# Optimization experiments

Measured on AMD Instinct MI355X. Metric: run time of the kernel, lower is better.

The kernel has to match this reference:

```python
import jax, jax.numpy as jnp
import numpy as np

D_MODEL = 128


def setup_inputs() -> dict:
    key = jax.random.key(0)
    ks = jax.random.split(key, 7)
    d = D_MODEL
    B, N = 4, 512
    # Kaiming-ish init scales for linear layers
    W1 = jax.random.normal(ks[0], (2 * d, d), jnp.float32) / np.sqrt(2 * d)
    b1 = jnp.zeros((d,), jnp.float32)
    W2 = jax.random.normal(ks[1], (d, d // 2), jnp.float32) / np.sqrt(d)
    b2 = jnp.zeros((d // 2,), jnp.float32)
    W3 = jax.random.normal(ks[2], (d // 2, 1), jnp.float32) / np.sqrt(d // 2)
    b3 = jnp.zeros((1,), jnp.float32)
    node_features = jax.random.normal(ks[3], (B, N, d), jnp.float32)
    return {"node_features": node_features, "W1": W1, "b1": b1,
            "W2": W2, "b2": b2, "W3": W3, "b3": b3}


def reference(node_features, W1, b1, W2, b2, W3, b3):
    # node_features: [B, N, d]. Pairwise concat [x_i, x_j] @ W1 is split as
    # x_i @ W1[:d] + x_j @ W1[d:] — same math as cat+Linear, but avoids
    # materializing the [B, N, N, 2d] concat tensor.
    d = node_features.shape[-1]
    hi = jnp.einsum('bnd,dk->bnk', node_features, W1[:d])   # [B, N, d]
    hj = jnp.einsum('bnd,dk->bnk', node_features, W1[d:])   # [B, N, d]
    h = jax.nn.relu(hi[:, :, None, :] + hj[:, None, :, :] + b1)  # [B, N, N, d]
    h = jax.nn.relu(jnp.einsum('bijk,km->bijm', h, W2) + b2)      # [B, N, N, d/2]
    logits = jnp.einsum('bijm,mo->bijo', h, W3) + b3              # [B, N, N, 1]
    return jax.nn.sigmoid(logits[..., 0])                          # [B, N, N]
```

## Files before the change

### kernel.cpp

```cpp
#include <hip/hip_runtime.h>
#include <hip/hip_fp16.h>

#define D_MODEL 128
#define NB 4
#define NN 512

typedef _Float16 f16;
typedef _Float16 f16x8 __attribute__((ext_vector_type(8)));
typedef float f32x4 __attribute__((ext_vector_type(4)));

__global__ __launch_bounds__(256) void prep_kernel(
    const float* __restrict__ x,
    const float* __restrict__ W1,
    const float* __restrict__ b1,
    const float* __restrict__ W2,
    f16* __restrict__ Hi, f16* __restrict__ Hj, f16* __restrict__ W2p)
{
    const int blk = blockIdx.x;
    const int t = threadIdx.x;
    if (blk < 256) {
        const int r0 = blk * 8;
        __shared__ float xs[8][128];
        for (int idx = t; idx < 8 * 128; idx += 256)
            xs[idx >> 7][idx & 127] = x[(size_t)r0 * 128 + idx];
        __syncthreads();

        const int isJ = t >> 7;
        const int k = t & 127;
        const float* wcol = W1 + (isJ ? 128 * 128 : 0) + k;
        float acc[8];
        #pragma unroll
        for (int r = 0; r < 8; r++) acc[r] = 0.f;
        for (int d = 0; d < 128; d++) {
            float w = wcol[d * 128];
            #pragma unroll
            for (int r = 0; r < 8; r++) acc[r] = fmaf(xs[r][d], w, acc[r]);
        }
        const float bb = isJ ? 0.f : b1[k];
        f16* dst = isJ ? Hj : Hi;
        #pragma unroll
        for (int r = 0; r < 8; r++)
            dst[(size_t)(r0 + r) * 128 + k] = (f16)(acc[r] + bb);
    } else {
        for (int slot = t; slot < 16 * 64; slot += 256) {
            const int lane = slot & 63;
            const int fidx = slot >> 6;
            const int kt = fidx >> 2, nt = fidx & 3;
            const int krow = kt * 32 + 8 * (lane >> 4);
            const int col = nt * 16 + (lane & 15);
            #pragma unroll
            for (int j = 0; j < 8; j++)
                W2p[(size_t)slot * 8 + j] = (f16)W2[(krow + j) * 64 + col];
        }
    }
}

__global__ __launch_bounds__(256, 4) void pair_kernel(
    const f16* __restrict__ Hi, const f16* __restrict__ Hj,
    const f16* __restrict__ W2p,
    const float* __restrict__ b2, const float* __restrict__ W3,
    const float* __restrict__ b3p, float* __restrict__ out)
{
    const int lane = threadIdx.x & 63;
    const int wave = threadIdx.x >> 6;
    const int bid = blockIdx.x;
    const int jg4 = bid & 7;
    const int ic  = (bid >> 3) & 31;
    const int b   = bid >> 8;
    const int j0 = (jg4 * 4 + wave) * 16;
    const int i0 = ic * 16;

    const int lrow = lane & 15;
    const int lgrp = lane >> 4;

    f16x8 w2f[4][4];
    #pragma unroll
    for (int kt = 0; kt < 4; kt++)
        #pragma unroll
        for (int nt = 0; nt < 4; nt++)
            w2f[kt][nt] = *(const f16x8*)(W2p + (size_t)((kt * 4 + nt) * 64 + lane) * 8);

    const f16* hjbase = Hj + (size_t)(b * NN + j0 + lrow) * 128 + 8 * lgrp;
    f16x8 hjf[4];
    #pragma unroll
    for (int kt = 0; kt < 4; kt++)
        hjf[kt] = *(const f16x8*)(hjbase + kt * 32);

    f32x4 b2v[4], w3v[4];
    #pragma unroll
    for (int nt = 0; nt < 4; nt++) {
        b2v[nt] = *(const f32x4*)(b2 + nt * 16 + 4 * lgrp);
        w3v[nt] = *(const f32x4*)(W3 + nt * 16 + 4 * lgrp);
    }
    const float b3 = b3p[0];

    const f16* hibase = Hi + (size_t)(b * NN + i0) * 128 + 8 * lgrp;
    float* orow = out + ((size_t)b * NN + i0) * NN + j0 + lrow;

    const f16x8 zero8 = (f16x8)(f16)0;

    #pragma unroll 2
    for (int ii = 0; ii < 16; ii++) {
        f16x8 hif[4];
        #pragma unroll
        for (int kt = 0; kt < 4; kt++)
            hif[kt] = *(const f16x8*)(hibase + ii * 128 + kt * 32);

        f32x4 accD[4];
        #pragma unroll
        for (int nt = 0; nt < 4; nt++) accD[nt] = (f32x4)(0.0f);

        #pragma unroll
        for (int kt = 0; kt < 4; kt++) {
            f16x8 s = hif[kt] + hjf[kt];
            s = __builtin_elementwise_max(s, zero8);
            #pragma unroll
            for (int nt = 0; nt < 4; nt++)
                accD[nt] = __builtin_amdgcn_mfma_f32_16x16x32_f16(w2f[kt][nt], s, accD[nt], 0, 0, 0);
        }

        float acc = 0.f;
        #pragma unroll
        for (int nt = 0; nt < 4; nt++) {
            #pragma unroll
            for (int r = 0; r < 4; r++) {
                float h = fmaxf(accD[nt][r] + b2v[nt][r], 0.f);
                acc = fmaf(h, w3v[nt][r], acc);
            }
        }
        acc += __shfl_xor(acc, 16, 64);
        acc += __shfl_xor(acc, 32, 64);
        float sg = __builtin_amdgcn_rcpf(1.f + __expf(-(acc + b3)));
        if (lgrp == 0)
            orow[(size_t)ii * NN] = sg;
    }
}

extern "C" void kernel_launch(void* const* d_in, const int* in_sizes, int n_in,
                              void* d_out, int out_size, void* d_ws, size_t ws_size,
                              hipStream_t stream) {
    const float* x  = (const float*)d_in[0];
    const float* W1 = (const float*)d_in[1];
    const float* b1 = (const float*)d_in[2];
    const float* W2 = (const float*)d_in[3];
    const float* b2 = (const float*)d_in[4];
    const float* W3 = (const float*)d_in[5];
    const float* b3 = (const float*)d_in[6];
    float* out = (float*)d_out;

    f16* Hi  = (f16*)d_ws;
    f16* Hj  = Hi + (size_t)NB * NN * 128;
    f16* W2p = Hj + (size_t)NB * NN * 128;

    prep_kernel<<<257, 256, 0, stream>>>(x, W1, b1, W2, Hi, Hj, W2p);
    pair_kernel<<<1024, 256, 0, stream>>>(Hi, Hj, W2p, b2, W3, b3, out);
}
```

Measured before the change: 123.0 us.

## Stage pair outputs in LDS for coalesced stores, remap blocks, vectorize prep loads

The pair kernel now writes each wave's sigmoid results into a shared 16x65 tile. After a barrier, the block stores full 64-float row segments with 16-byte vector stores, replacing scattered 64-byte per-wave row writes. Block indices are permuted so that consecutive hardware blocks map to different batch and row groups, which changes scheduling and cache locality. The prep kernel reads the x tile from LDS as float4 vectors and unrolls the reduction loop. The padded 65-float row stride makes the float4 LDS reads misaligned on odd rows, which risks slower or incorrect accesses.

Result: no change. 121.5 us (-1.2%).

```diff
diff --git a/kernel.cpp b/kernel.cpp
--- a/kernel.cpp
+++ b/kernel.cpp
@@ -21,6 +21,7 @@
     if (blk < 256) {
         const int r0 = blk * 8;
         __shared__ float xs[8][128];
+        #pragma unroll
         for (int idx = t; idx < 8 * 128; idx += 256)
             xs[idx >> 7][idx & 127] = x[(size_t)r0 * 128 + idx];
         __syncthreads();
@@ -28,13 +29,18 @@
         const int isJ = t >> 7;
         const int k = t & 127;
         const float* wcol = W1 + (isJ ? 128 * 128 : 0) + k;
-        float acc[8];
-        #pragma unroll
-        for (int r = 0; r < 8; r++) acc[r] = 0.f;
-        for (int d = 0; d < 128; d++) {
-            float w = wcol[d * 128];
+        float acc[8] = {0.f, 0.f, 0.f, 0.f, 0.f, 0.f, 0.f, 0.f};
+        #pragma unroll 4
+        for (int d4 = 0; d4 < 32; d4++) {
+            f32x4 xv[8];
             #pragma unroll
-            for (int r = 0; r < 8; r++) acc[r] = fmaf(xs[r][d], w, acc[r]);
+            for (int r = 0; r < 8; r++) xv[r] = *(const f32x4*)&xs[r][d4 * 4];
+            #pragma unroll
+            for (int dd = 0; dd < 4; dd++) {
+                float w = wcol[(d4 * 4 + dd) * 128];
+                #pragma unroll
+                for (int r = 0; r < 8; r++) acc[r] = fmaf(xv[r][dd], w, acc[r]);
+            }
         }
         const float bb = isJ ? 0.f : b1[k];
         f16* dst = isJ ? Hj : Hi;
@@ -63,15 +69,19 @@
 {
     const int lane = threadIdx.x & 63;
     const int wave = threadIdx.x >> 6;
-    const int bid = blockIdx.x;
-    const int jg4 = bid & 7;
-    const int ic  = (bid >> 3) & 31;
-    const int b   = bid >> 8;
-    const int j0 = (jg4 * 4 + wave) * 16;
+
+    const int logical = (blockIdx.x & 7) * 128 + (blockIdx.x >> 3);
+    const int jg = logical & 7;
+    const int ic = (logical >> 3) & 31;
+    const int b  = logical >> 8;
+    const int jblk = jg * 64;
+    const int j0 = jblk + wave * 16;
     const int i0 = ic * 16;
 
     const int lrow = lane & 15;
     const int lgrp = lane >> 4;
+
+    __shared__ float tile[16][65];
 
     f16x8 w2f[4][4];
     #pragma unroll
@@ -95,7 +105,6 @@
     const float b3 = b3p[0];
 
     const f16* hibase = Hi + (size_t)(b * NN + i0) * 128 + 8 * lgrp;
-    float* orow = out + ((size_t)b * NN + i0) * NN + j0 + lrow;
 
     const f16x8 zero8 = (f16x8)(f16)0;
 
@@ -132,7 +141,16 @@
         acc += __shfl_xor(acc, 32, 64);
         float sg = __builtin_amdgcn_rcpf(1.f + __expf(-(acc + b3)));
         if (lgrp == 0)
-            orow[(size_t)ii * NN] = sg;
+            tile[ii][wave * 16 + lrow] = sg;
+    }
+
+    __syncthreads();
+
+    {
+        const int row = threadIdx.x >> 4;
+        const int c4  = threadIdx.x & 15;
+        f32x4 v = *(const f32x4*)&tile[row][c4 * 4];
+        *(f32x4*)(out + ((size_t)(b * NN + i0 + row)) * NN + jblk + c4 * 4) = v;
     }
 }
 
```
